# Kernel tuning notes

Hardware: AMD Instinct MI355X
Metric: run time of the kernel (lower is better)

Reference implementation:

```python
import jax, jax.numpy as jnp
import numpy as np

N, K, IN_DIM, OUT_DIM = 131072, 16, 256, 128


def setup_inputs() -> dict:
    key = jax.random.key(0)
    ks = jax.random.split(key, 6)
    s1 = 1.0 / np.sqrt(IN_DIM)
    s2 = 1.0 / np.sqrt(OUT_DIM)
    return {
        "x": jax.random.normal(ks[0], (N, IN_DIM), dtype=jnp.float32),
        "z": jax.random.randint(ks[1], (N,), 0, K, dtype=jnp.int32),
        "W1": jax.random.uniform(ks[2], (K, IN_DIM, OUT_DIM), jnp.float32, -s1, s1),
        "b1": jax.random.uniform(ks[3], (K, OUT_DIM), jnp.float32, -s1, s1),
        "W2": jax.random.uniform(ks[4], (K, OUT_DIM, 2), jnp.float32, -s2, s2),
        "b2": jax.random.uniform(ks[5], (K, 2), jnp.float32, -s2, s2),
    }


def reference(x, z, W1, b1, W2, b2):
    # Per-cluster expert MLP: tokens with z==i go through expert i.
    # Loop over the fixed, small number of experts (k); data dims stay vectorized.
    k = W1.shape[0]
    ri = jnp.zeros((x.shape[0], 2), dtype=x.dtype)
    for i in range(k):
        h = jax.nn.relu(x @ W1[i] + b1[i])          # [N, out_dim]
        logits = h @ W2[i] + b2[i]                  # [N, 2]
        ri = jnp.where((z == i)[:, None], logits, ri)
    # Every z in [0, k) is covered, so every row of ri has been written
    # (matches the torch path where non-empty clusters overwrite -inf).
    return jax.nn.softmax(ri, axis=-1)
```

## Files before the change

### kernel.cpp

```cpp
#include <hip/hip_runtime.h>
#include <hip/hip_bf16.h>

#define KEXP   16
#define IN_DIM 256
#define OUT_DIM 128
#define TILE   128
#define BPE    16

typedef float f32x4 __attribute__((ext_vector_type(4)));
typedef short bf16x8 __attribute__((ext_vector_type(8)));
typedef const unsigned int __attribute__((address_space(1)))* gptr_t;
typedef unsigned int __attribute__((address_space(3)))* lptr_t;

__device__ __forceinline__ ushort f2bf(float f) {
    union { float f; unsigned u; } v; v.f = f;
    return (ushort)((v.u + 0x7fffu + ((v.u >> 16) & 1u)) >> 16);
}

__global__ __launch_bounds__(256) void prep_k(const float* __restrict__ W1,
                                              ushort* __restrict__ w1t,
                                              const int* __restrict__ z,
                                              int* __restrict__ counts, int n) {
    __shared__ float ld[64][65];
    int bid = blockIdx.x, tid = threadIdx.x;
    if (bid < 128) {
        int e = bid >> 3, sub = bid & 7;
        int k0 = (sub & 3) * 64, n0 = (sub >> 2) * 64;
        const float* src = W1 + (long)e * (IN_DIM * OUT_DIM);
        int tr = tid >> 6, tc = tid & 63;
#pragma unroll
        for (int i = 0; i < 16; i++) {
            int row = i * 4 + tr;
            ld[row][tc] = src[(k0 + row) * OUT_DIM + n0 + tc];
        }
        __syncthreads();
        char* dst = (char*)w1t + (long)e * (OUT_DIM * IN_DIM * 2);
#pragma unroll
        for (int i = 0; i < 16; i++) {
            int col = n0 + i * 4 + tr;
            int L = (col * IN_DIM + k0 + tc) * 2;
            int S = L ^ ((col & 7) << 4);
            *(ushort*)(dst + S) = f2bf(ld[tc][i * 4 + tr]);
        }
    } else {
        int* h = (int*)ld;
        if (tid < KEXP) h[tid] = 0;
        __syncthreads();
        for (int i = (bid - 128) * 256 + tid; i < n; i += 256 * 256)
            atomicAdd(&h[z[i]], 1);
        __syncthreads();
        if (tid < KEXP) atomicAdd(&counts[tid], h[tid]);
    }
}

__global__ void scan_k(const int* __restrict__ counts, int* __restrict__ bases) {
    if (threadIdx.x == 0) {
        int acc = 0;
        for (int i = 0; i < KEXP; i++) { bases[i] = acc; acc += counts[i]; }
    }
}

__global__ __launch_bounds__(256) void scatter_k(const int* __restrict__ z,
                                                 const int* __restrict__ bases,
                                                 int* __restrict__ cursors,
                                                 int* __restrict__ perm, int n) {
    __shared__ int lc[KEXP];
    __shared__ int lb[KEXP];
    int tid = threadIdx.x;
    if (tid < KEXP) lc[tid] = 0;
    __syncthreads();
    int i = blockIdx.x * 256 + tid;
    int e = 0, r = 0;
    if (i < n) {
        e = z[i];
        r = atomicAdd(&lc[e], 1);
    }
    __syncthreads();
    if (tid < KEXP && lc[tid] > 0) lb[tid] = atomicAdd(&cursors[tid], lc[tid]);
    __syncthreads();
    if (i < n) perm[bases[e] + lb[e] + r] = i;
}

__global__ __launch_bounds__(512, 2) void mlp_k(
    const float* __restrict__ x, const float* __restrict__ b1,
    const float* __restrict__ W2, const float* __restrict__ b2,
    const int* __restrict__ counts, const int* __restrict__ bases,
    const int* __restrict__ perm, const ushort* __restrict__ w1t,
    float* __restrict__ out) {
    __shared__ char Wl[65536];
    __shared__ char Al[65536];

    int b = blockIdx.x;
    int e = b >> 4, slot = b & 15;
    int cnt = counts[e];
    int pb0 = bases[e];
    int ntiles = (cnt + TILE - 1) / TILE;

    int tid = threadIdx.x;
    int lane = tid & 63, w = tid >> 6;
    int li = lane & 15, q = lane >> 4;

    const char* wsrc = (const char*)w1t + (long)e * (OUT_DIM * IN_DIM * 2);
#pragma unroll
    for (int i = 0; i < 8; i++) {
        int off = w * 8192 + i * 1024;
        __builtin_amdgcn_global_load_lds((gptr_t)(wsrc + off + lane * 16),
                                         (lptr_t)(Wl + off), 16, 0, 0);
    }

    float bbv[8], w2a[8], w2b[8];
#pragma unroll
    for (int nn = 0; nn < 8; nn++) {
        int col = nn * 16 + li;
        bbv[nn] = b1[e * OUT_DIM + col];
        w2a[nn] = W2[(e * OUT_DIM + col) * 2 + 0];
        w2b[nn] = W2[(e * OUT_DIM + col) * 2 + 1];
    }
    float bb0 = b2[e * 2 + 0], bb1 = b2[e * 2 + 1];

    f32x4 av[16];
    int pb_cur = 0, nr_cur = 0;
    if (slot < ntiles) {
        pb_cur = pb0 + slot * TILE;
        nr_cur = cnt - slot * TILE;
        int rr = w * 16 + li;
        int pv = perm[pb_cur + (rr < nr_cur ? rr : nr_cur - 1)];
#pragma unroll
        for (int i = 0; i < 16; i++) {
            int g = __shfl(pv, i, 16);
            av[i] = *(const f32x4*)((const char*)x + (long)g * 1024 + lane * 16);
        }
    }

    for (int t = slot; t < ntiles; t += BPE) {
#pragma unroll
        for (int i = 0; i < 16; i++) {
            int r = w * 16 + i;
            uint2 pk;
            pk.x = (unsigned)f2bf(av[i][0]) | ((unsigned)f2bf(av[i][1]) << 16);
            pk.y = (unsigned)f2bf(av[i][2]) | ((unsigned)f2bf(av[i][3]) << 16);
            *(uint2*)(Al + r * 512 + ((lane * 8) ^ ((r & 7) << 4))) = pk;
        }
        __syncthreads();

        int tn = t + BPE;
        int pb_nx = 0, nr_nx = 0;
        if (tn < ntiles) {
            pb_nx = pb0 + tn * TILE;
            nr_nx = cnt - tn * TILE;
            int rr = w * 16 + li;
            int pv = perm[pb_nx + (rr < nr_nx ? rr : nr_nx - 1)];
#pragma unroll
            for (int i = 0; i < 16; i++) {
                int g = __shfl(pv, i, 16);
                av[i] = *(const f32x4*)((const char*)x + (long)g * 1024 + lane * 16);
            }
        }

        f32x4 acc[8];
#pragma unroll
        for (int nn = 0; nn < 8; nn++) acc[nn] = (f32x4)0.0f;

        int arow = w * 16 + li;
        int aswz = (arow & 7) << 4;
#pragma unroll
        for (int kk = 0; kk < 8; kk++) {
            bf16x8 af = *(const bf16x8*)(Al + arow * 512 + ((kk * 64 + q * 16) ^ aswz));
#pragma unroll
            for (int nn = 0; nn < 8; nn++) {
                int col = nn * 16 + li;
                bf16x8 bf = *(const bf16x8*)(Wl + col * 512 + ((kk * 64 + q * 16) ^ ((col & 7) << 4)));
                acc[nn] = __builtin_amdgcn_mfma_f32_16x16x32_bf16(af, bf, acc[nn], 0, 0, 0);
            }
        }

        float p0[4] = {0.f, 0.f, 0.f, 0.f}, p1[4] = {0.f, 0.f, 0.f, 0.f};
#pragma unroll
        for (int nn = 0; nn < 8; nn++) {
#pragma unroll
            for (int r = 0; r < 4; r++) {
                float h = fmaxf(acc[nn][r] + bbv[nn], 0.0f);
                p0[r] += h * w2a[nn];
                p1[r] += h * w2b[nn];
            }
        }
#pragma unroll
        for (int m = 1; m < 16; m <<= 1)
#pragma unroll
            for (int r = 0; r < 4; r++) {
                p0[r] += __shfl_xor(p0[r], m, 64);
                p1[r] += __shfl_xor(p1[r], m, 64);
            }
        if (li == 0) {
#pragma unroll
            for (int r = 0; r < 4; r++) {
                int mm = w * 16 + q * 4 + r;
                if (mm < nr_cur) {
                    int orig = perm[pb_cur + mm];
                    float l0 = p0[r] + bb0, l1 = p1[r] + bb1;
                    float mx = fmaxf(l0, l1);
                    float e0 = __expf(l0 - mx), e1 = __expf(l1 - mx);
                    float inv = 1.0f / (e0 + e1);
                    *(float2*)(out + (long)orig * 2) = make_float2(e0 * inv, e1 * inv);
                }
            }
        }
        __syncthreads();
        pb_cur = pb_nx;
        nr_cur = nr_nx;
    }
}

extern "C" void kernel_launch(void* const* d_in, const int* in_sizes, int n_in,
                              void* d_out, int out_size, void* d_ws, size_t ws_size,
                              hipStream_t stream) {
    const float* x  = (const float*)d_in[0];
    const int*   z  = (const int*)d_in[1];
    const float* W1 = (const float*)d_in[2];
    const float* b1 = (const float*)d_in[3];
    const float* W2 = (const float*)d_in[4];
    const float* b2 = (const float*)d_in[5];
    float* out = (float*)d_out;
    int n = in_sizes[1];

    int* counts  = (int*)d_ws;
    int* cursors = counts + 16;
    int* basesp  = counts + 32;
    int* perm    = counts + 256;
    ushort* w1t  = (ushort*)((char*)d_ws + 1024 + (size_t)n * 4);

    hipMemsetAsync(counts, 0, 128, stream);
    prep_k<<<384, 256, 0, stream>>>(W1, w1t, z, counts, n);
    scan_k<<<1, 64, 0, stream>>>(counts, basesp);
    scatter_k<<<(n + 255) / 256, 256, 0, stream>>>(z, basesp, cursors, perm, n);
    mlp_k<<<KEXP * BPE, 512, 0, stream>>>(x, b1, W2, b2, counts, basesp, perm, w1t, out);
}
```

Baseline: 228.7 us.

## Replace global permutation with per-chunk local sort and fragment-layout weights

Drops the global histogram, scan and scatter kernels. Each block now takes a contiguous chunk of 128 tokens, sorts them by expert in shared memory, and runs 16-row MFMA tiles per expert, so x is read coalesced and the launch count shrinks. W1 is pre-packed into an MFMA fragment layout and read straight from global/L2 instead of being staged in LDS, which lets 4 blocks fit per CU. In exchange, the many partial 16-row tiles waste MFMA work, and the weight fragments are re-read from L2 by every block.

```diff
diff --git a/kernel.cpp b/kernel.cpp
--- a/kernel.cpp
+++ b/kernel.cpp
@@ -1,16 +1,14 @@
 #include <hip/hip_runtime.h>
 #include <hip/hip_bf16.h>
 
-#define KEXP   16
-#define IN_DIM 256
+#define KEXP    16
+#define IN_DIM  256
 #define OUT_DIM 128
-#define TILE   128
-#define BPE    16
+#define CHUNK   128
+#define MAXT    24
 
 typedef float f32x4 __attribute__((ext_vector_type(4)));
 typedef short bf16x8 __attribute__((ext_vector_type(8)));
-typedef const unsigned int __attribute__((address_space(1)))* gptr_t;
-typedef unsigned int __attribute__((address_space(3)))* lptr_t;
 
 __device__ __forceinline__ ushort f2bf(float f) {
     union { float f; unsigned u; } v; v.f = f;
@@ -18,158 +16,107 @@
 }
 
 __global__ __launch_bounds__(256) void prep_k(const float* __restrict__ W1,
-                                              ushort* __restrict__ w1t,
-                                              const int* __restrict__ z,
-                                              int* __restrict__ counts, int n) {
+                                              ushort* __restrict__ w1frag) {
     __shared__ float ld[64][65];
     int bid = blockIdx.x, tid = threadIdx.x;
-    if (bid < 128) {
-        int e = bid >> 3, sub = bid & 7;
-        int k0 = (sub & 3) * 64, n0 = (sub >> 2) * 64;
-        const float* src = W1 + (long)e * (IN_DIM * OUT_DIM);
-        int tr = tid >> 6, tc = tid & 63;
+    int e = bid >> 3, sub = bid & 7;
+    int k0 = (sub & 3) * 64, n0 = (sub >> 2) * 64;
+    const float* src = W1 + (long)e * (IN_DIM * OUT_DIM);
+    int tr = tid >> 6, tc = tid & 63;
 #pragma unroll
-        for (int i = 0; i < 16; i++) {
-            int row = i * 4 + tr;
-            ld[row][tc] = src[(k0 + row) * OUT_DIM + n0 + tc];
-        }
-        __syncthreads();
-        char* dst = (char*)w1t + (long)e * (OUT_DIM * IN_DIM * 2);
+    for (int i = 0; i < 16; i++)
+        ld[i * 4 + tr][tc] = src[(k0 + i * 4 + tr) * OUT_DIM + n0 + tc];
+    __syncthreads();
 #pragma unroll
-        for (int i = 0; i < 16; i++) {
-            int col = n0 + i * 4 + tr;
-            int L = (col * IN_DIM + k0 + tc) * 2;
-            int S = L ^ ((col & 7) << 4);
-            *(ushort*)(dst + S) = f2bf(ld[tc][i * 4 + tr]);
-        }
-    } else {
-        int* h = (int*)ld;
-        if (tid < KEXP) h[tid] = 0;
-        __syncthreads();
-        for (int i = (bid - 128) * 256 + tid; i < n; i += 256 * 256)
-            atomicAdd(&h[z[i]], 1);
-        __syncthreads();
-        if (tid < KEXP) atomicAdd(&counts[tid], h[tid]);
+    for (int i = 0; i < 16; i++) {
+        int col = n0 + i * 4 + tr;
+        int k   = k0 + tc;
+        int kk = k >> 5, q = (k >> 3) & 3, j = k & 7;
+        int li = col & 15, nn = col >> 4, lane = q * 16 + li;
+        long byte = ((((long)e * 8 + kk) * 8 + nn) * 64 + lane) * 16 + j * 2;
+        *(ushort*)((char*)w1frag + byte) = f2bf(ld[tc][i * 4 + tr]);
     }
 }
 
-__global__ void scan_k(const int* __restrict__ counts, int* __restrict__ bases) {
-    if (threadIdx.x == 0) {
-        int acc = 0;
-        for (int i = 0; i < KEXP; i++) { bases[i] = acc; acc += counts[i]; }
-    }
-}
-
-__global__ __launch_bounds__(256) void scatter_k(const int* __restrict__ z,
-                                                 const int* __restrict__ bases,
-                                                 int* __restrict__ cursors,
-                                                 int* __restrict__ perm, int n) {
-    __shared__ int lc[KEXP];
-    __shared__ int lb[KEXP];
-    int tid = threadIdx.x;
-    if (tid < KEXP) lc[tid] = 0;
-    __syncthreads();
-    int i = blockIdx.x * 256 + tid;
-    int e = 0, r = 0;
-    if (i < n) {
-        e = z[i];
-        r = atomicAdd(&lc[e], 1);
-    }
-    __syncthreads();
-    if (tid < KEXP && lc[tid] > 0) lb[tid] = atomicAdd(&cursors[tid], lc[tid]);
-    __syncthreads();
-    if (i < n) perm[bases[e] + lb[e] + r] = i;
-}
-
-__global__ __launch_bounds__(512, 2) void mlp_k(
-    const float* __restrict__ x, const float* __restrict__ b1,
-    const float* __restrict__ W2, const float* __restrict__ b2,
-    const int* __restrict__ counts, const int* __restrict__ bases,
-    const int* __restrict__ perm, const ushort* __restrict__ w1t,
-    float* __restrict__ out) {
-    __shared__ char Wl[65536];
-    __shared__ char Al[65536];
-
-    int b = blockIdx.x;
-    int e = b >> 4, slot = b & 15;
-    int cnt = counts[e];
-    int pb0 = bases[e];
-    int ntiles = (cnt + TILE - 1) / TILE;
+__global__ __launch_bounds__(512, 4) void moe_k(
+    const float* __restrict__ x, const int* __restrict__ z,
+    const float* __restrict__ b1, const float* __restrict__ W2,
+    const float* __restrict__ b2, const ushort* __restrict__ w1frag,
+    float* __restrict__ out, int n) {
+    __shared__ __align__(16) char Al[CHUNK * 512];
+    __shared__ int lrow[CHUNK];
+    __shared__ int lorig[CHUNK];
+    __shared__ int hist[KEXP], cur[KEXP];
+    __shared__ int t_e[MAXT], t_row[MAXT], t_cnt[MAXT];
+    __shared__ int ntile_s;
 
     int tid = threadIdx.x;
     int lane = tid & 63, w = tid >> 6;
     int li = lane & 15, q = lane >> 4;
+    int chunk0 = blockIdx.x * CHUNK;
 
-    const char* wsrc = (const char*)w1t + (long)e * (OUT_DIM * IN_DIM * 2);
+    if (tid < KEXP) hist[tid] = 0;
+    __syncthreads();
+    int e_t = -1;
+    if (tid < CHUNK) {
+        e_t = z[chunk0 + tid];
+        atomicAdd(&hist[e_t], 1);
+    }
+    __syncthreads();
+    if (tid == 0) {
+        int a = 0, nt = 0;
+        for (int e = 0; e < KEXP; e++) {
+            int c = hist[e];
+            cur[e] = a;
+            for (int j = 0; j < c; j += 16) {
+                t_e[nt] = e; t_row[nt] = a + j; t_cnt[nt] = min(16, c - j); nt++;
+            }
+            a += c;
+        }
+        ntile_s = nt;
+    }
+    __syncthreads();
+    if (tid < CHUNK) {
+        int r = atomicAdd(&cur[e_t], 1);
+        lrow[tid] = r;
+        lorig[r] = chunk0 + tid;
+    }
+    __syncthreads();
+
+    int lr[16];
 #pragma unroll
-    for (int i = 0; i < 8; i++) {
-        int off = w * 8192 + i * 1024;
-        __builtin_amdgcn_global_load_lds((gptr_t)(wsrc + off + lane * 16),
-                                         (lptr_t)(Wl + off), 16, 0, 0);
+    for (int i = 0; i < 16; i++) lr[i] = lrow[i * 8 + w];
+#pragma unroll
+    for (int i = 0; i < 16; i++) {
+        int row = i * 8 + w;
+        f32x4 v = *(const f32x4*)(x + ((long)chunk0 + row) * IN_DIM + lane * 4);
+        uint2 pk;
+        pk.x = (unsigned)f2bf(v[0]) | ((unsigned)f2bf(v[1]) << 16);
+        pk.y = (unsigned)f2bf(v[2]) | ((unsigned)f2bf(v[3]) << 16);
+        int r = lr[i];
+        *(uint2*)(Al + r * 512 + ((lane * 8) ^ ((r & 7) << 4))) = pk;
     }
+    __syncthreads();
 
-    float bbv[8], w2a[8], w2b[8];
-#pragma unroll
-    for (int nn = 0; nn < 8; nn++) {
-        int col = nn * 16 + li;
-        bbv[nn] = b1[e * OUT_DIM + col];
-        w2a[nn] = W2[(e * OUT_DIM + col) * 2 + 0];
-        w2b[nn] = W2[(e * OUT_DIM + col) * 2 + 1];
-    }
-    float bb0 = b2[e * 2 + 0], bb1 = b2[e * 2 + 1];
+    int ntile = ntile_s;
+    for (int ti = w; ti < ntile; ti += 8) {
+        int e = t_e[ti], rbase = t_row[ti], cnt = t_cnt[ti];
 
-    f32x4 av[16];
-    int pb_cur = 0, nr_cur = 0;
-    if (slot < ntiles) {
-        pb_cur = pb0 + slot * TILE;
-        nr_cur = cnt - slot * TILE;
-        int rr = w * 16 + li;
-        int pv = perm[pb_cur + (rr < nr_cur ? rr : nr_cur - 1)];
-#pragma unroll
-        for (int i = 0; i < 16; i++) {
-            int g = __shfl(pv, i, 16);
-            av[i] = *(const f32x4*)((const char*)x + (long)g * 1024 + lane * 16);
-        }
-    }
+        int arow = rbase + (li < cnt ? li : cnt - 1);
+        int aswz = (arow & 7) << 4;
 
-    for (int t = slot; t < ntiles; t += BPE) {
-#pragma unroll
-        for (int i = 0; i < 16; i++) {
-            int r = w * 16 + i;
-            uint2 pk;
-            pk.x = (unsigned)f2bf(av[i][0]) | ((unsigned)f2bf(av[i][1]) << 16);
-            pk.y = (unsigned)f2bf(av[i][2]) | ((unsigned)f2bf(av[i][3]) << 16);
-            *(uint2*)(Al + r * 512 + ((lane * 8) ^ ((r & 7) << 4))) = pk;
-        }
-        __syncthreads();
-
-        int tn = t + BPE;
-        int pb_nx = 0, nr_nx = 0;
-        if (tn < ntiles) {
-            pb_nx = pb0 + tn * TILE;
-            nr_nx = cnt - tn * TILE;
-            int rr = w * 16 + li;
-            int pv = perm[pb_nx + (rr < nr_nx ? rr : nr_nx - 1)];
-#pragma unroll
-            for (int i = 0; i < 16; i++) {
-                int g = __shfl(pv, i, 16);
-                av[i] = *(const f32x4*)((const char*)x + (long)g * 1024 + lane * 16);
-            }
-        }
+        const char* wf = (const char*)w1frag + ((long)e * 64) * 1024 + lane * 16;
 
         f32x4 acc[8];
 #pragma unroll
         for (int nn = 0; nn < 8; nn++) acc[nn] = (f32x4)0.0f;
 
-        int arow = w * 16 + li;
-        int aswz = (arow & 7) << 4;
 #pragma unroll
         for (int kk = 0; kk < 8; kk++) {
             bf16x8 af = *(const bf16x8*)(Al + arow * 512 + ((kk * 64 + q * 16) ^ aswz));
 #pragma unroll
             for (int nn = 0; nn < 8; nn++) {
-                int col = nn * 16 + li;
-                bf16x8 bf = *(const bf16x8*)(Wl + col * 512 + ((kk * 64 + q * 16) ^ ((col & 7) << 4)));
+                bf16x8 bf = *(const bf16x8*)(wf + (long)(kk * 8 + nn) * 1024);
                 acc[nn] = __builtin_amdgcn_mfma_f32_16x16x32_bf16(af, bf, acc[nn], 0, 0, 0);
             }
         }
@@ -177,11 +124,15 @@
         float p0[4] = {0.f, 0.f, 0.f, 0.f}, p1[4] = {0.f, 0.f, 0.f, 0.f};
 #pragma unroll
         for (int nn = 0; nn < 8; nn++) {
+            int col = nn * 16 + li;
+            float bb = b1[e * OUT_DIM + col];
+            float wa = W2[(e * OUT_DIM + col) * 2 + 0];
+            float wb = W2[(e * OUT_DIM + col) * 2 + 1];
 #pragma unroll
             for (int r = 0; r < 4; r++) {
-                float h = fmaxf(acc[nn][r] + bbv[nn], 0.0f);
-                p0[r] += h * w2a[nn];
-                p1[r] += h * w2b[nn];
+                float h = fmaxf(acc[nn][r] + bb, 0.0f);
+                p0[r] += h * wa;
+                p1[r] += h * wb;
             }
         }
 #pragma unroll
@@ -192,11 +143,12 @@
                 p1[r] += __shfl_xor(p1[r], m, 64);
             }
         if (li == 0) {
+            float bb0 = b2[e * 2 + 0], bb1 = b2[e * 2 + 1];
 #pragma unroll
             for (int r = 0; r < 4; r++) {
-                int mm = w * 16 + q * 4 + r;
-                if (mm < nr_cur) {
-                    int orig = perm[pb_cur + mm];
+                int m = q * 4 + r;
+                if (m < cnt) {
+                    int orig = lorig[rbase + m];
                     float l0 = p0[r] + bb0, l1 = p1[r] + bb1;
                     float mx = fmaxf(l0, l1);
                     float e0 = __expf(l0 - mx), e1 = __expf(l1 - mx);
@@ -205,9 +157,6 @@
                 }
             }
         }
-        __syncthreads();
-        pb_cur = pb_nx;
-        nr_cur = nr_nx;
     }
 }
 
@@ -223,15 +172,8 @@
     float* out = (float*)d_out;
     int n = in_sizes[1];
 
-    int* counts  = (int*)d_ws;
-    int* cursors = counts + 16;
-    int* basesp  = counts + 32;
-    int* perm    = counts + 256;
-    ushort* w1t  = (ushort*)((char*)d_ws + 1024 + (size_t)n * 4);
+    ushort* w1frag = (ushort*)d_ws;
 
-    hipMemsetAsync(counts, 0, 128, stream);
-    prep_k<<<384, 256, 0, stream>>>(W1, w1t, z, counts, n);
-    scan_k<<<1, 64, 0, stream>>>(counts, basesp);
-    scatter_k<<<(n + 255) / 256, 256, 0, stream>>>(z, basesp, cursors, perm, n);
-    mlp_k<<<KEXP * BPE, 512, 0, stream>>>(x, b1, W2, b2, counts, basesp, perm, w1t, out);
+    prep_k<<<128, 256, 0, stream>>>(W1, w1frag);
+    moe_k<<<n / CHUNK, 512, 0, stream>>>(x, z, b1, W2, b2, w1frag, out, n);
 }
```

Measured after the change: 268.3 us. 1.17x slower.
